# Kernel tuning notes

Measured on AMD Instinct MI355X. Metric: run time of the kernel, lower is better.

Reference implementation:

```python
import jax, jax.numpy as jnp
import numpy as np

B, N, D = 2, 1024, 1024
H, DH = 16, 64          # nhead, head_dim (D = H*DH)
FF = 4096               # dim_feedforward = 4*D
E = 8                   # num experts
EPS = 1e-5


def layer_norm(x, s, b):
    m = jnp.mean(x, -1, keepdims=True)
    v = jnp.mean((x - m) ** 2, -1, keepdims=True)
    return (x - m) * jax.lax.rsqrt(v + EPS) * s + b


def moe_gate(x, Wg):
    # top-1 gating: expert index + gate probability per token
    probs = jax.nn.softmax(x @ Wg, axis=-1)            # [B,N,E]
    idx = jnp.argmax(probs, axis=-1)                   # [B,N]
    gw = jnp.take_along_axis(probs, idx[..., None], -1)[..., 0]  # [B,N]
    return idx, gw


def moe_linear(x, W, b, idx, gw):
    # x:[B,N,Din], W:[E,Din,Dout], b:[E,Dout]; route each token to expert idx
    y = jnp.einsum('bnd,edh->bneh', x, W) + b          # [B,N,E,Dout]
    oh = jax.nn.one_hot(idx, E, dtype=x.dtype)         # [B,N,E]
    return jnp.einsum('bneh,bne->bnh', y, oh) * gw[..., None]


def setup_inputs() -> dict:
    key = jax.random.key(0)
    ks = jax.random.split(key, 8)
    g = lambda k, shape, sc: jax.random.normal(k, shape, jnp.float32) * sc
    inv_d = 1.0 / np.sqrt(D)
    return dict(
        src=g(ks[0], (B, N, D), 1.0),
        key_padding_mask=jnp.zeros((B, N), dtype=bool),
        Wg_attn=g(ks[1], (D, E), inv_d),
        Wqkv=g(ks[2], (E, D, 3 * D), inv_d), bqkv=jnp.zeros((E, 3 * D), jnp.float32),
        Wo=g(ks[3], (E, D, D), inv_d), bo=jnp.zeros((E, D), jnp.float32),
        Wg_ffn=g(ks[4], (D, E), inv_d),
        W1=g(ks[5], (E, D, FF), inv_d), b1=jnp.zeros((E, FF), jnp.float32),
        W2=g(ks[6], (E, FF, D), 1.0 / np.sqrt(FF)), b2=jnp.zeros((E, D), jnp.float32),
        ln1_s=jnp.ones((D,), jnp.float32), ln1_b=jnp.zeros((D,), jnp.float32),
        ln2_s=jnp.ones((D,), jnp.float32), ln2_b=jnp.zeros((D,), jnp.float32),
    )


def reference(src, key_padding_mask, Wg_attn, Wqkv, bqkv, Wo, bo,
              Wg_ffn, W1, b1, W2, b2, ln1_s, ln1_b, ln2_s, ln2_b):
    # attention mask: key_padding_mask.unsqueeze(1).unsqueeze(1) * -10000
    mask = jnp.where(key_padding_mask[:, None, None, :], -10000.0, 0.0).astype(src.dtype)

    # --- MoE self-attention (gate decided once, reused for qkv and dense) ---
    idx, gw = moe_gate(src, Wg_attn)
    qkv = moe_linear(src, Wqkv, bqkv, idx, gw)                 # [B,N,3D]
    q, k, v = jnp.split(qkv, 3, axis=-1)
    heads = lambda t: t.reshape(B, N, H, DH).transpose(0, 2, 1, 3)  # [B,H,N,DH]
    q, k, v = heads(q), heads(k), heads(v)
    scores = jnp.einsum('bhqd,bhkd->bhqk', q, k) / np.sqrt(DH) + mask
    probs = jax.nn.softmax(scores, axis=-1)
    ctx = jnp.einsum('bhqk,bhkd->bhqd', probs, v)
    ctx = ctx.transpose(0, 2, 1, 3).reshape(B, N, D)
    attn_out = moe_linear(ctx, Wo, bo, idx, gw)

    # post-norm residual
    x = layer_norm(src + attn_out, ln1_s, ln1_b)

    # --- MoE FFN (its own gate, shared across both linears) ---
    fidx, fgw = moe_gate(x, Wg_ffn)
    h = jax.nn.gelu(moe_linear(x, W1, b1, fidx, fgw))
    ffn = moe_linear(h, W2, b2, fidx, fgw)

    return layer_norm(x + ffn, ln2_s, ln2_b)
```

## Files before the change

kernel.cpp:

```cpp
#include <hip/hip_runtime.h>


#define B_   2
#define N_   1024
#define D_   1024
#define H_   16
#define DH_  64
#define FF_  4096
#define E_   8
#define NTOK 2048

typedef __attribute__((ext_vector_type(8))) short short8;
typedef __attribute__((ext_vector_type(8))) unsigned short ushort8;
typedef __attribute__((ext_vector_type(4))) float f32x4;

__device__ inline unsigned short f2bf(float f) {
  unsigned u = __float_as_uint(f);
  u += 0x7FFFu + ((u >> 16) & 1u);
  return (unsigned short)(u >> 16);
}

__device__ inline float gelu_tanh(float x) {
  float x3 = x * x * x;
  float t = tanhf(0.7978845608028654f * (x + 0.044715f * x3));
  return 0.5f * x * (1.0f + t);
}

__global__ __launch_bounds__(256) void gate_kernel(
    const float* __restrict__ X, const float* __restrict__ Wg,
    int* __restrict__ idx, float* __restrict__ gwv, int* __restrict__ cnt) {
  int t = blockIdx.x * 4 + (threadIdx.x >> 6);
  int lane = threadIdx.x & 63;
  const float* x = X + (size_t)t * D_;
  float acc[E_];
#pragma unroll
  for (int j = 0; j < E_; j++) acc[j] = 0.f;
#pragma unroll
  for (int i = 0; i < 16; i++) {
    int d = i * 64 + lane;
    float xv = x[d];
    const float4* w = (const float4*)(Wg + (size_t)d * E_);
    float4 w0 = w[0], w1 = w[1];
    acc[0] += xv * w0.x; acc[1] += xv * w0.y; acc[2] += xv * w0.z; acc[3] += xv * w0.w;
    acc[4] += xv * w1.x; acc[5] += xv * w1.y; acc[6] += xv * w1.z; acc[7] += xv * w1.w;
  }
#pragma unroll
  for (int o = 1; o < 64; o <<= 1) {
#pragma unroll
    for (int j = 0; j < E_; j++) acc[j] += __shfl_xor(acc[j], o, 64);
  }
  float m = acc[0]; int bi = 0;
#pragma unroll
  for (int j = 1; j < E_; j++) { if (acc[j] > m) { m = acc[j]; bi = j; } }
  float den = 0.f;
#pragma unroll
  for (int j = 0; j < E_; j++) den += expf(acc[j] - m);
  float gw = expf(acc[bi] - m) / den;
  if (lane == 0) { idx[t] = bi; gwv[t] = gw; atomicAdd(&cnt[bi], 1); }
}

__global__ __launch_bounds__(256) void route_kernel(
    const int* __restrict__ idx, const int* __restrict__ cnt,
    int* __restrict__ off, int* __restrict__ perm, int ntok) {
  __shared__ int loff[E_ + 1];
  __shared__ int lfill[E_];
  if (threadIdx.x == 0) {
    int s = 0;
    for (int e = 0; e < E_; e++) { loff[e] = s; s += cnt[e]; }
    loff[E_] = s;
  }
  if (threadIdx.x < E_) lfill[threadIdx.x] = 0;
  __syncthreads();
  for (int t = (int)threadIdx.x; t < ntok; t += 256) {
    int e = idx[t];
    int p = atomicAdd(&lfill[e], 1);
    perm[loff[e] + p] = t;
  }
  if (threadIdx.x < E_ + 1) off[threadIdx.x] = loff[threadIdx.x];
}

__global__ __launch_bounds__(256) void transpose_w_kernel(
    const float* __restrict__ W, unsigned short* __restrict__ WT, int K, int N) {
  __shared__ float T[64][68];
  int e = blockIdx.z;
  int n0 = blockIdx.x * 64, k0 = blockIdx.y * 64;
  int tid = threadIdx.x;
  {
    int kr = tid >> 4;
    int nc = (tid & 15) * 4;
#pragma unroll
    for (int j = 0; j < 4; j++) {
      int k = kr + j * 16;
      float4 v = *(const float4*)(W + ((size_t)e * K + k0 + k) * N + n0 + nc);
      *(float4*)&T[k][nc] = v;
    }
  }
  __syncthreads();
  {
    int n = tid >> 2;
    int ko = (tid & 3) * 16;
    ushort8 o0, o1;
#pragma unroll
    for (int i = 0; i < 8; i++) o0[i] = f2bf(T[ko + i][n]);
#pragma unroll
    for (int i = 0; i < 8; i++) o1[i] = f2bf(T[ko + 8 + i][n]);
    unsigned short* p = WT + ((size_t)e * N + n0 + n) * K + k0 + ko;
    *(ushort8*)p = o0;
    *(ushort8*)(p + 8) = o1;
  }
}

template <typename AT, bool GELU, bool OBF16>
__global__ __launch_bounds__(256) void gemm_kernel(
    const AT* __restrict__ A, int ldA,
    const unsigned short* __restrict__ WT, const float* __restrict__ bias,
    const float* __restrict__ gwv, const int* __restrict__ perm, const int* __restrict__ off,
    void* __restrict__ out, int ldO, int K, int N) {
  __shared__ __align__(16) unsigned short As[128][40];
  __shared__ __align__(16) unsigned short Bs[128][40];
  __shared__ int toks[128];
  __shared__ float gws[128];

  int e = blockIdx.y;
  int base = off[e];
  int cnt = off[e + 1] - base;
  int m0 = blockIdx.z * 128;
  if (m0 >= cnt) return;
  int rows_valid = min(128, cnt - m0);
  int tid = threadIdx.x;
  if (tid < 128) {
    int r = (tid < rows_valid) ? tid : (rows_valid - 1);
    int t = perm[base + m0 + r];
    toks[tid] = t;
    gws[tid] = gwv[t];
  }
  int nb = blockIdx.x * 128;
  int lane = tid & 63, wave = tid >> 6;
  int wm = (wave >> 1) * 64, wn = (wave & 1) * 64;
  int lr = lane & 15, lg = lane >> 4;
  f32x4 acc[4][4];
#pragma unroll
  for (int m = 0; m < 4; m++)
#pragma unroll
    for (int n = 0; n < 4; n++) acc[m][n] = (f32x4){0.f, 0.f, 0.f, 0.f};
  int srow = tid >> 1, koff = (tid & 1) * 16;
  __syncthreads();

  for (int k0 = 0; k0 < K; k0 += 32) {
    {
      const AT* ar = A + (size_t)toks[srow] * ldA + k0 + koff;
      ushort8 o0, o1;
      if constexpr (sizeof(AT) == 4) {
        const float* fa = (const float*)ar;
        float4 v0 = *(const float4*)(fa);
        float4 v1 = *(const float4*)(fa + 4);
        float4 v2 = *(const float4*)(fa + 8);
        float4 v3 = *(const float4*)(fa + 12);
        o0[0] = f2bf(v0.x); o0[1] = f2bf(v0.y); o0[2] = f2bf(v0.z); o0[3] = f2bf(v0.w);
        o0[4] = f2bf(v1.x); o0[5] = f2bf(v1.y); o0[6] = f2bf(v1.z); o0[7] = f2bf(v1.w);
        o1[0] = f2bf(v2.x); o1[1] = f2bf(v2.y); o1[2] = f2bf(v2.z); o1[3] = f2bf(v2.w);
        o1[4] = f2bf(v3.x); o1[5] = f2bf(v3.y); o1[6] = f2bf(v3.z); o1[7] = f2bf(v3.w);
      } else {
        o0 = *(const ushort8*)ar;
        o1 = *(const ushort8*)(ar + 8);
      }
      *(ushort8*)&As[srow][koff] = o0;
      *(ushort8*)&As[srow][koff + 8] = o1;
      const unsigned short* br = WT + ((size_t)e * N + nb + srow) * K + k0 + koff;
      *(ushort8*)&Bs[srow][koff] = *(const ushort8*)br;
      *(ushort8*)&Bs[srow][koff + 8] = *(const ushort8*)(br + 8);
    }
    __syncthreads();
    short8 av[4], bv[4];
#pragma unroll
    for (int m = 0; m < 4; m++) av[m] = *(const short8*)&As[wm + m * 16 + lr][lg * 8];
#pragma unroll
    for (int n = 0; n < 4; n++) bv[n] = *(const short8*)&Bs[wn + n * 16 + lr][lg * 8];
#pragma unroll
    for (int m = 0; m < 4; m++)
#pragma unroll
      for (int n = 0; n < 4; n++)
        acc[m][n] = __builtin_amdgcn_mfma_f32_16x16x32_bf16(av[m], bv[n], acc[m][n], 0, 0, 0);
    __syncthreads();
  }

#pragma unroll
  for (int n = 0; n < 4; n++) {
    int col = wn + n * 16 + lr;
    float bvs = bias[(size_t)e * N + nb + col];
#pragma unroll
    for (int m = 0; m < 4; m++) {
#pragma unroll
      for (int reg = 0; reg < 4; reg++) {
        int r = wm + m * 16 + lg * 4 + reg;
        if (r < rows_valid) {
          int t = toks[r];
          float val = (acc[m][n][reg] + bvs) * gws[r];
          if constexpr (GELU) val = gelu_tanh(val);
          if constexpr (OBF16)
            ((unsigned short*)out)[(size_t)t * ldO + nb + col] = f2bf(val);
          else
            ((float*)out)[(size_t)t * ldO + nb + col] = val;
        }
      }
    }
  }
}

__global__ __launch_bounds__(256) void vtrans_kernel(
    const unsigned short* __restrict__ qkv, unsigned short* __restrict__ vT) {
  __shared__ __align__(16) unsigned short T[64][72];
  int bh = blockIdx.x;
  int b = bh >> 4, h = bh & 15;
  int tile = blockIdx.y;
  int tid = threadIdx.x;
  {
    int tk = tid >> 2, dof = (tid & 3) * 16;
    const unsigned short* p =
        qkv + ((size_t)(b * N_ + tile * 64 + tk)) * 3072 + 2048 + h * 64 + dof;
    *(ushort8*)&T[tk][dof] = *(const ushort8*)p;
    *(ushort8*)&T[tk][dof + 8] = *(const ushort8*)(p + 8);
  }
  __syncthreads();
  {
    int dh = tid >> 2, tof = (tid & 3) * 16;
    ushort8 o0, o1;
#pragma unroll
    for (int i = 0; i < 8; i++) o0[i] = T[tof + i][dh];
#pragma unroll
    for (int i = 0; i < 8; i++) o1[i] = T[tof + 8 + i][dh];
    unsigned short* q = vT + ((size_t)bh * 64 + dh) * N_ + tile * 64 + tof;
    *(ushort8*)q = o0;
    *(ushort8*)(q + 8) = o1;
  }
}

__global__ __launch_bounds__(256) void attn_kernel(
    const unsigned short* __restrict__ qkv, const unsigned short* __restrict__ vT,
    const unsigned char* __restrict__ kpm, unsigned short* __restrict__ ctx) {
  __shared__ __align__(16) unsigned short Qs[64][72];
  __shared__ __align__(16) unsigned short Ks[64][72];
  __shared__ __align__(16) unsigned short Vs[64][72];
  __shared__ __align__(16) unsigned short Ps[4][16][72];
  __shared__ float maskf[64];
  int qt = blockIdx.x, bh = blockIdx.y;
  int b = bh >> 4, h = bh & 15;
  int tid = threadIdx.x, lane = tid & 63, wave = tid >> 6;
  int lr = lane & 15, lg = lane >> 4;
  {
    int r = tid >> 2, dof = (tid & 3) * 16;
    const unsigned short* p = qkv + ((size_t)(b * N_ + qt * 64 + r)) * 3072 + h * 64 + dof;
    *(ushort8*)&Qs[r][dof] = *(const ushort8*)p;
    *(ushort8*)&Qs[r][dof + 8] = *(const ushort8*)(p + 8);
  }
  __syncthreads();
  short8 aq[2];
  aq[0] = *(const short8*)&Qs[wave * 16 + lr][lg * 8];
  aq[1] = *(const short8*)&Qs[wave * 16 + lr][32 + lg * 8];
  f32x4 O[4];
  float mrun[4], lrun[4];
#pragma unroll
  for (int r = 0; r < 4; r++) { mrun[r] = -1e30f; lrun[r] = 0.f; O[r] = (f32x4){0.f, 0.f, 0.f, 0.f}; }

  for (int kt = 0; kt < 16; kt++) {
    __syncthreads();
    {
      int r = tid >> 2, dof = (tid & 3) * 16;
      const unsigned short* p =
          qkv + ((size_t)(b * N_ + kt * 64 + r)) * 3072 + 1024 + h * 64 + dof;
      *(ushort8*)&Ks[r][dof] = *(const ushort8*)p;
      *(ushort8*)&Ks[r][dof + 8] = *(const ushort8*)(p + 8);
      const unsigned short* pv = vT + ((size_t)bh * 64 + r) * N_ + kt * 64 + dof;
      *(ushort8*)&Vs[r][dof] = *(const ushort8*)pv;
      *(ushort8*)&Vs[r][dof + 8] = *(const ushort8*)(pv + 8);
      if (tid < 64) maskf[tid] = kpm[b * N_ + kt * 64 + tid] ? -10000.f : 0.f;
    }
    __syncthreads();
    f32x4 S[4];
#pragma unroll
    for (int n = 0; n < 4; n++) {
      f32x4 s = (f32x4){0.f, 0.f, 0.f, 0.f};
#pragma unroll
      for (int ks = 0; ks < 2; ks++) {
        short8 bk = *(const short8*)&Ks[n * 16 + lr][ks * 32 + lg * 8];
        s = __builtin_amdgcn_mfma_f32_16x16x32_bf16(aq[ks], bk, s, 0, 0, 0);
      }
      float mv = maskf[n * 16 + lr];
#pragma unroll
      for (int r = 0; r < 4; r++) s[r] = s[r] * 0.125f + mv;
      S[n] = s;
    }
    float cur[4];
#pragma unroll
    for (int r = 0; r < 4; r++)
      cur[r] = fmaxf(fmaxf(S[0][r], S[1][r]), fmaxf(S[2][r], S[3][r]));
#pragma unroll
    for (int o = 1; o < 16; o <<= 1) {
#pragma unroll
      for (int r = 0; r < 4; r++) cur[r] = fmaxf(cur[r], __shfl_xor(cur[r], o, 64));
    }
    float alpha[4], rsum[4];
#pragma unroll
    for (int r = 0; r < 4; r++) {
      float mn = fmaxf(mrun[r], cur[r]);
      alpha[r] = expf(mrun[r] - mn);
      mrun[r] = mn;
      rsum[r] = 0.f;
    }
#pragma unroll
    for (int n = 0; n < 4; n++) {
#pragma unroll
      for (int r = 0; r < 4; r++) {
        S[n][r] = expf(S[n][r] - mrun[r]);
        rsum[r] += S[n][r];
      }
    }
#pragma unroll
    for (int o = 1; o < 16; o <<= 1) {
#pragma unroll
      for (int r = 0; r < 4; r++) rsum[r] += __shfl_xor(rsum[r], o, 64);
    }
#pragma unroll
    for (int r = 0; r < 4; r++) lrun[r] = lrun[r] * alpha[r] + rsum[r];
#pragma unroll
    for (int d = 0; d < 4; d++)
#pragma unroll
      for (int r = 0; r < 4; r++) O[d][r] *= alpha[r];
#pragma unroll
    for (int n = 0; n < 4; n++)
#pragma unroll
      for (int r = 0; r < 4; r++) Ps[wave][lg * 4 + r][n * 16 + lr] = f2bf(S[n][r]);
    short8 pf[2];
    pf[0] = *(const short8*)&Ps[wave][lr][lg * 8];
    pf[1] = *(const short8*)&Ps[wave][lr][32 + lg * 8];
#pragma unroll
    for (int d = 0; d < 4; d++) {
#pragma unroll
      for (int ks = 0; ks < 2; ks++) {
        short8 bv = *(const short8*)&Vs[d * 16 + lr][ks * 32 + lg * 8];
        O[d] = __builtin_amdgcn_mfma_f32_16x16x32_bf16(pf[ks], bv, O[d], 0, 0, 0);
      }
    }
  }
#pragma unroll
  for (int r = 0; r < 4; r++) lrun[r] = 1.f / lrun[r];
#pragma unroll
  for (int d = 0; d < 4; d++) {
#pragma unroll
    for (int r = 0; r < 4; r++) {
      int q = qt * 64 + wave * 16 + lg * 4 + r;
      int dh = d * 16 + lr;
      ctx[((size_t)(b * N_ + q)) * D_ + h * DH_ + dh] = f2bf(O[d][r] * lrun[r]);
    }
  }
}

__global__ __launch_bounds__(256) void ln_kernel(
    const float* __restrict__ A, const float* __restrict__ Bv,
    const float* __restrict__ S, const float* __restrict__ Bi, float* __restrict__ O) {
  int t = blockIdx.x, tid = threadIdx.x;
  float4 va = ((const float4*)(A + (size_t)t * D_))[tid];
  float4 vb = ((const float4*)(Bv + (size_t)t * D_))[tid];
  float4 v;
  v.x = va.x + vb.x; v.y = va.y + vb.y; v.z = va.z + vb.z; v.w = va.w + vb.w;
  float s = v.x + v.y + v.z + v.w;
  float sq = v.x * v.x + v.y * v.y + v.z * v.z + v.w * v.w;
#pragma unroll
  for (int o = 1; o < 64; o <<= 1) {
    s += __shfl_xor(s, o, 64);
    sq += __shfl_xor(sq, o, 64);
  }
  __shared__ float ss[4], ssq[4];
  int wave = tid >> 6, lane = tid & 63;
  if (lane == 0) { ss[wave] = s; ssq[wave] = sq; }
  __syncthreads();
  float ts = ss[0] + ss[1] + ss[2] + ss[3];
  float tsq = ssq[0] + ssq[1] + ssq[2] + ssq[3];
  float mean = ts * (1.f / D_);
  float var = tsq * (1.f / D_) - mean * mean;
  float rs = rsqrtf(var + 1e-5f);
  float4 sv = ((const float4*)S)[tid];
  float4 bv = ((const float4*)Bi)[tid];
  float4 o;
  o.x = (v.x - mean) * rs * sv.x + bv.x;
  o.y = (v.y - mean) * rs * sv.y + bv.y;
  o.z = (v.z - mean) * rs * sv.z + bv.z;
  o.w = (v.w - mean) * rs * sv.w + bv.w;
  ((float4*)(O + (size_t)t * D_))[tid] = o;
}

extern "C" void kernel_launch(void* const* d_in, const int* in_sizes, int n_in,
                              void* d_out, int out_size, void* d_ws, size_t ws_size,
                              hipStream_t stream) {
  (void)in_sizes; (void)n_in; (void)out_size; (void)ws_size;
  const float* src     = (const float*)d_in[0];
  const unsigned char* kpm = (const unsigned char*)d_in[1];
  const float* Wg_attn = (const float*)d_in[2];
  const float* Wqkv    = (const float*)d_in[3];
  const float* bqkv    = (const float*)d_in[4];
  const float* Wo      = (const float*)d_in[5];
  const float* bo      = (const float*)d_in[6];
  const float* Wg_ffn  = (const float*)d_in[7];
  const float* W1      = (const float*)d_in[8];
  const float* b1      = (const float*)d_in[9];
  const float* W2      = (const float*)d_in[10];
  const float* b2      = (const float*)d_in[11];
  const float* ln1_s   = (const float*)d_in[12];
  const float* ln1_b   = (const float*)d_in[13];
  const float* ln2_s   = (const float*)d_in[14];
  const float* ln2_b   = (const float*)d_in[15];
  float* out = (float*)d_out;

  char* ws = (char*)d_ws;
  size_t o = 0;
  auto alloc = [&](size_t bytes) -> void* {
    void* p = ws + o;
    o += (bytes + 255) & ~(size_t)255;
    return p;
  };
  int* meta = (int*)alloc(256);
  int* cnt1 = meta;
  int* off1 = meta + 8;
  int* cnt2 = meta + 17;
  int* off2 = meta + 25;
  int* idx1 = (int*)alloc(NTOK * 4);
  float* gw1 = (float*)alloc(NTOK * 4);
  int* perm1 = (int*)alloc(NTOK * 4);
  int* idx2 = (int*)alloc(NTOK * 4);
  float* gw2 = (float*)alloc(NTOK * 4);
  int* perm2 = (int*)alloc(NTOK * 4);
  unsigned short* WT = (unsigned short*)alloc((size_t)E_ * FF_ * D_ * 2);
  unsigned short* qkvb = (unsigned short*)alloc((size_t)NTOK * 3072 * 2);
  unsigned short* vT = (unsigned short*)alloc((size_t)32 * 64 * N_ * 2);
  unsigned short* hbuf = qkvb;
  unsigned short* ctx = (unsigned short*)alloc((size_t)NTOK * D_ * 2);
  float* attn_out = (float*)alloc((size_t)NTOK * D_ * 4);
  float* ffn = attn_out;
  float* x = (float*)alloc((size_t)NTOK * D_ * 4);

  hipMemsetAsync(meta, 0, 256, stream);

  gate_kernel<<<512, 256, 0, stream>>>(src, Wg_attn, idx1, gw1, cnt1);
  route_kernel<<<1, 256, 0, stream>>>(idx1, cnt1, off1, perm1, NTOK);
  transpose_w_kernel<<<dim3(3072 / 64, 1024 / 64, 8), 256, 0, stream>>>(Wqkv, WT, 1024, 3072);
  gemm_kernel<float, false, true><<<dim3(3072 / 128, 8, 16), 256, 0, stream>>>(
      src, 1024, WT, bqkv, gw1, perm1, off1, qkvb, 3072, 1024, 3072);
  vtrans_kernel<<<dim3(32, 16), 256, 0, stream>>>(qkvb, vT);
  attn_kernel<<<dim3(16, 32), 256, 0, stream>>>(qkvb, vT, kpm, ctx);
  transpose_w_kernel<<<dim3(1024 / 64, 1024 / 64, 8), 256, 0, stream>>>(Wo, WT, 1024, 1024);
  gemm_kernel<unsigned short, false, false><<<dim3(1024 / 128, 8, 16), 256, 0, stream>>>(
      ctx, 1024, WT, bo, gw1, perm1, off1, attn_out, 1024, 1024, 1024);
  ln_kernel<<<NTOK, 256, 0, stream>>>(src, attn_out, ln1_s, ln1_b, x);

  gate_kernel<<<512, 256, 0, stream>>>(x, Wg_ffn, idx2, gw2, cnt2);
  route_kernel<<<1, 256, 0, stream>>>(idx2, cnt2, off2, perm2, NTOK);
  transpose_w_kernel<<<dim3(4096 / 64, 1024 / 64, 8), 256, 0, stream>>>(W1, WT, 1024, 4096);
  gemm_kernel<float, true, true><<<dim3(4096 / 128, 8, 16), 256, 0, stream>>>(
      x, 1024, WT, b1, gw2, perm2, off2, hbuf, 4096, 1024, 4096);
  transpose_w_kernel<<<dim3(1024 / 64, 4096 / 64, 8), 256, 0, stream>>>(W2, WT, 4096, 1024);
  gemm_kernel<unsigned short, false, false><<<dim3(1024 / 128, 8, 16), 256, 0, stream>>>(
      hbuf, 4096, WT, b2, gw2, perm2, off2, ffn, 1024, 4096, 1024);
  ln_kernel<<<NTOK, 256, 0, stream>>>(x, ffn, ln2_s, ln2_b, out);
}
```

Before: 779.1 us.

## Split-K expert GEMMs with separate reduce epilogues fused into layernorm

The expert GEMMs now split the K dimension across extra grid blocks (2-way for QKV/W1, 4-way for Wo/W2) and write fp32 partial sums. Separate reduce kernels add the partials, then apply bias, gate weight, GELU and the bf16 cast. For the two output projections, the reduction is fused into the residual+layernorm kernel. This raises block count to fill the GPU when routed tiles are few, at the cost of extra fp32 partial traffic and extra launches. The transpose-write thread mapping is also changed for better coalescing.

```diff
diff --git a/kernel.cpp b/kernel.cpp
--- a/kernel.cpp
+++ b/kernel.cpp
@@ -12,6 +12,7 @@
 
 typedef __attribute__((ext_vector_type(8))) short short8;
 typedef __attribute__((ext_vector_type(8))) unsigned short ushort8;
+typedef __attribute__((ext_vector_type(4))) unsigned short ushort4v;
 typedef __attribute__((ext_vector_type(4))) float f32x4;
 
 __device__ inline unsigned short f2bf(float f) {
@@ -97,8 +98,8 @@
   }
   __syncthreads();
   {
-    int n = tid >> 2;
-    int ko = (tid & 3) * 16;
+    int n = tid & 63;
+    int ko = (tid >> 6) * 16;
     ushort8 o0, o1;
 #pragma unroll
     for (int i = 0; i < 8; i++) o0[i] = f2bf(T[ko + i][n]);
@@ -110,29 +111,28 @@
   }
 }
 
-template <typename AT, bool GELU, bool OBF16>
+template <typename AT, int KS>
 __global__ __launch_bounds__(256) void gemm_kernel(
     const AT* __restrict__ A, int ldA,
-    const unsigned short* __restrict__ WT, const float* __restrict__ bias,
-    const float* __restrict__ gwv, const int* __restrict__ perm, const int* __restrict__ off,
-    void* __restrict__ out, int ldO, int K, int N) {
+    const unsigned short* __restrict__ WT,
+    const int* __restrict__ perm, const int* __restrict__ off,
+    float* __restrict__ part, int K, int N) {
   __shared__ __align__(16) unsigned short As[128][40];
   __shared__ __align__(16) unsigned short Bs[128][40];
   __shared__ int toks[128];
-  __shared__ float gws[128];
 
   int e = blockIdx.y;
   int base = off[e];
   int cnt = off[e + 1] - base;
-  int m0 = blockIdx.z * 128;
+  int mt = blockIdx.z / KS;
+  int kc = blockIdx.z % KS;
+  int m0 = mt * 128;
   if (m0 >= cnt) return;
   int rows_valid = min(128, cnt - m0);
   int tid = threadIdx.x;
   if (tid < 128) {
     int r = (tid < rows_valid) ? tid : (rows_valid - 1);
-    int t = perm[base + m0 + r];
-    toks[tid] = t;
-    gws[tid] = gwv[t];
+    toks[tid] = perm[base + m0 + r];
   }
   int nb = blockIdx.x * 128;
   int lane = tid & 63, wave = tid >> 6;
@@ -144,9 +144,11 @@
 #pragma unroll
     for (int n = 0; n < 4; n++) acc[m][n] = (f32x4){0.f, 0.f, 0.f, 0.f};
   int srow = tid >> 1, koff = (tid & 1) * 16;
+  int KL = K / KS;
+  int kbeg = kc * KL;
   __syncthreads();
 
-  for (int k0 = 0; k0 < K; k0 += 32) {
+  for (int k0 = kbeg; k0 < kbeg + KL; k0 += 32) {
     {
       const AT* ar = A + (size_t)toks[srow] * ldA + k0 + koff;
       ushort8 o0, o1;
@@ -184,26 +186,51 @@
     __syncthreads();
   }
 
+  float* pr = part + (size_t)kc * ((size_t)NTOK * N);
 #pragma unroll
   for (int n = 0; n < 4; n++) {
-    int col = wn + n * 16 + lr;
-    float bvs = bias[(size_t)e * N + nb + col];
+    int col = nb + wn + n * 16 + lr;
 #pragma unroll
     for (int m = 0; m < 4; m++) {
 #pragma unroll
       for (int reg = 0; reg < 4; reg++) {
         int r = wm + m * 16 + lg * 4 + reg;
-        if (r < rows_valid) {
-          int t = toks[r];
-          float val = (acc[m][n][reg] + bvs) * gws[r];
-          if constexpr (GELU) val = gelu_tanh(val);
-          if constexpr (OBF16)
-            ((unsigned short*)out)[(size_t)t * ldO + nb + col] = f2bf(val);
-          else
-            ((float*)out)[(size_t)t * ldO + nb + col] = val;
-        }
+        if (r < rows_valid)
+          pr[(size_t)toks[r] * N + col] = acc[m][n][reg];
       }
     }
+  }
+}
+
+template <int KS, bool GELU, bool OBF16>
+__global__ __launch_bounds__(256) void reduce_kernel(
+    const float* __restrict__ part, const float* __restrict__ bias,
+    const float* __restrict__ gwv, const int* __restrict__ idx,
+    void* __restrict__ out, int N) {
+  int t = blockIdx.y;
+  int n = (blockIdx.x * 256 + threadIdx.x) * 4;
+  int e = idx[t];
+  float gw = gwv[t];
+  const float* p = part + (size_t)t * N + n;
+  float4 a = *(const float4*)p;
+#pragma unroll
+  for (int k = 1; k < KS; k++) {
+    float4 q = *(const float4*)(p + (size_t)k * NTOK * N);
+    a.x += q.x; a.y += q.y; a.z += q.z; a.w += q.w;
+  }
+  float4 bv = *(const float4*)(bias + (size_t)e * N + n);
+  a.x = (a.x + bv.x) * gw; a.y = (a.y + bv.y) * gw;
+  a.z = (a.z + bv.z) * gw; a.w = (a.w + bv.w) * gw;
+  if constexpr (GELU) {
+    a.x = gelu_tanh(a.x); a.y = gelu_tanh(a.y);
+    a.z = gelu_tanh(a.z); a.w = gelu_tanh(a.w);
+  }
+  if constexpr (OBF16) {
+    ushort4v o;
+    o[0] = f2bf(a.x); o[1] = f2bf(a.y); o[2] = f2bf(a.z); o[3] = f2bf(a.w);
+    *(ushort4v*)((unsigned short*)out + (size_t)t * N + n) = o;
+  } else {
+    *(float4*)((float*)out + (size_t)t * N + n) = a;
   }
 }
 
@@ -355,14 +382,30 @@
   }
 }
 
-__global__ __launch_bounds__(256) void ln_kernel(
-    const float* __restrict__ A, const float* __restrict__ Bv,
-    const float* __restrict__ S, const float* __restrict__ Bi, float* __restrict__ O) {
+template <int KS>
+__global__ __launch_bounds__(256) void ln_reduce_kernel(
+    const float* __restrict__ res, const float* __restrict__ part,
+    const float* __restrict__ bias, const float* __restrict__ gwv,
+    const int* __restrict__ idx,
+    const float* __restrict__ S, const float* __restrict__ Bi,
+    float* __restrict__ O) {
   int t = blockIdx.x, tid = threadIdx.x;
-  float4 va = ((const float4*)(A + (size_t)t * D_))[tid];
-  float4 vb = ((const float4*)(Bv + (size_t)t * D_))[tid];
+  int e = idx[t];
+  float gw = gwv[t];
+  const float* p = part + (size_t)t * D_ + tid * 4;
+  float4 a = *(const float4*)p;
+#pragma unroll
+  for (int k = 1; k < KS; k++) {
+    float4 q = *(const float4*)(p + (size_t)k * NTOK * D_);
+    a.x += q.x; a.y += q.y; a.z += q.z; a.w += q.w;
+  }
+  float4 bv4 = *(const float4*)(bias + (size_t)e * D_ + tid * 4);
+  float4 vr = ((const float4*)(res + (size_t)t * D_))[tid];
   float4 v;
-  v.x = va.x + vb.x; v.y = va.y + vb.y; v.z = va.z + vb.z; v.w = va.w + vb.w;
+  v.x = vr.x + (a.x + bv4.x) * gw;
+  v.y = vr.y + (a.y + bv4.y) * gw;
+  v.z = vr.z + (a.z + bv4.z) * gw;
+  v.w = vr.w + (a.w + bv4.w) * gw;
   float s = v.x + v.y + v.z + v.w;
   float sq = v.x * v.x + v.y * v.y + v.z * v.z + v.w * v.w;
 #pragma unroll
@@ -380,12 +423,12 @@
   float var = tsq * (1.f / D_) - mean * mean;
   float rs = rsqrtf(var + 1e-5f);
   float4 sv = ((const float4*)S)[tid];
-  float4 bv = ((const float4*)Bi)[tid];
+  float4 bi = ((const float4*)Bi)[tid];
   float4 o;
-  o.x = (v.x - mean) * rs * sv.x + bv.x;
-  o.y = (v.y - mean) * rs * sv.y + bv.y;
-  o.z = (v.z - mean) * rs * sv.z + bv.z;
-  o.w = (v.w - mean) * rs * sv.w + bv.w;
+  o.x = (v.x - mean) * rs * sv.x + bi.x;
+  o.y = (v.y - mean) * rs * sv.y + bi.y;
+  o.z = (v.z - mean) * rs * sv.z + bi.z;
+  o.w = (v.w - mean) * rs * sv.w + bi.w;
   ((float4*)(O + (size_t)t * D_))[tid] = o;
 }
 
@@ -434,31 +477,36 @@
   unsigned short* vT = (unsigned short*)alloc((size_t)32 * 64 * N_ * 2);
   unsigned short* hbuf = qkvb;
   unsigned short* ctx = (unsigned short*)alloc((size_t)NTOK * D_ * 2);
-  float* attn_out = (float*)alloc((size_t)NTOK * D_ * 4);
-  float* ffn = attn_out;
   float* x = (float*)alloc((size_t)NTOK * D_ * 4);
+  float* part = (float*)alloc((size_t)2 * NTOK * FF_ * 4);
 
   hipMemsetAsync(meta, 0, 256, stream);
 
   gate_kernel<<<512, 256, 0, stream>>>(src, Wg_attn, idx1, gw1, cnt1);
   route_kernel<<<1, 256, 0, stream>>>(idx1, cnt1, off1, perm1, NTOK);
   transpose_w_kernel<<<dim3(3072 / 64, 1024 / 64, 8), 256, 0, stream>>>(Wqkv, WT, 1024, 3072);
-  gemm_kernel<float, false, true><<<dim3(3072 / 128, 8, 16), 256, 0, stream>>>(
-      src, 1024, WT, bqkv, gw1, perm1, off1, qkvb, 3072, 1024, 3072);
+  gemm_kernel<float, 2><<<dim3(3072 / 128, 8, 32), 256, 0, stream>>>(
+      src, 1024, WT, perm1, off1, part, 1024, 3072);
+  reduce_kernel<2, false, true><<<dim3(3, NTOK), 256, 0, stream>>>(
+      part, bqkv, gw1, idx1, qkvb, 3072);
   vtrans_kernel<<<dim3(32, 16), 256, 0, stream>>>(qkvb, vT);
   attn_kernel<<<dim3(16, 32), 256, 0, stream>>>(qkvb, vT, kpm, ctx);
   transpose_w_kernel<<<dim3(1024 / 64, 1024 / 64, 8), 256, 0, stream>>>(Wo, WT, 1024, 1024);
-  gemm_kernel<unsigned short, false, false><<<dim3(1024 / 128, 8, 16), 256, 0, stream>>>(
-      ctx, 1024, WT, bo, gw1, perm1, off1, attn_out, 1024, 1024, 1024);
-  ln_kernel<<<NTOK, 256, 0, stream>>>(src, attn_out, ln1_s, ln1_b, x);
+  gemm_kernel<unsigned short, 4><<<dim3(1024 / 128, 8, 64), 256, 0, stream>>>(
+      ctx, 1024, WT, perm1, off1, part, 1024, 1024);
+  ln_reduce_kernel<4><<<NTOK, 256, 0, stream>>>(
+      src, part, bo, gw1, idx1, ln1_s, ln1_b, x);
 
   gate_kernel<<<512, 256, 0, stream>>>(x, Wg_ffn, idx2, gw2, cnt2);
   route_kernel<<<1, 256, 0, stream>>>(idx2, cnt2, off2, perm2, NTOK);
   transpose_w_kernel<<<dim3(4096 / 64, 1024 / 64, 8), 256, 0, stream>>>(W1, WT, 1024, 4096);
-  gemm_kernel<float, true, true><<<dim3(4096 / 128, 8, 16), 256, 0, stream>>>(
-      x, 1024, WT, b1, gw2, perm2, off2, hbuf, 4096, 1024, 4096);
+  gemm_kernel<float, 2><<<dim3(4096 / 128, 8, 32), 256, 0, stream>>>(
+      x, 1024, WT, perm2, off2, part, 1024, 4096);
+  reduce_kernel<2, true, true><<<dim3(4, NTOK), 256, 0, stream>>>(
+      part, b1, gw2, idx2, hbuf, 4096);
   transpose_w_kernel<<<dim3(1024 / 64, 4096 / 64, 8), 256, 0, stream>>>(W2, WT, 4096, 1024);
-  gemm_kernel<unsigned short, false, false><<<dim3(1024 / 128, 8, 16), 256, 0, stream>>>(
-      hbuf, 4096, WT, b2, gw2, perm2, off2, ffn, 1024, 4096, 1024);
-  ln_kernel<<<NTOK, 256, 0, stream>>>(x, ffn, ln2_s, ln2_b, out);
-}
+  gemm_kernel<unsigned short, 4><<<dim3(1024 / 128, 8, 64), 256, 0, stream>>>(
+      hbuf, 4096, WT, perm2, off2, part, 4096, 1024);
+  ln_reduce_kernel<4><<<NTOK, 256, 0, stream>>>(
+      x, part, b2, gw2, idx2, ln2_s, ln2_b, out);
+}
```

Result: faster. 748.2 us (-4.0%).
